# Performance work log

Measured on AMD Instinct MI355X. Metric: run time of the kernel, lower is better.

The kernel has to match this reference:

```python
import jax, jax.numpy as jnp
import numpy as np

B, S, E, H, FF = 4, 2048, 1024, 16, 4096
TD = 32  # transition_dim


def _layer_norm(v, g, b, eps=1e-5):
    m = v.mean(-1, keepdims=True)
    var = ((v - m) ** 2).mean(-1, keepdims=True)
    return (v - m) * jax.lax.rsqrt(var + eps) * g + b


def setup_inputs() -> dict:
    key = jax.random.key(0)
    ks = jax.random.split(key, 8)
    w = 0.02
    return {
        "x": jax.random.normal(ks[0], (B, S, E), dtype=jnp.float32),
        "transition_dim": TD,
        "ln1_g": jnp.ones((E,), jnp.float32),
        "ln1_b": jnp.zeros((E,), jnp.float32),
        "ln2_g": jnp.ones((E,), jnp.float32),
        "ln2_b": jnp.zeros((E,), jnp.float32),
        "w_qkv": jax.random.normal(ks[1], (3 * E, E), jnp.float32) * w,
        "b_qkv": jnp.zeros((3 * E,), jnp.float32),
        "w_o": jax.random.normal(ks[2], (E, E), jnp.float32) * w,
        "b_o": jnp.zeros((E,), jnp.float32),
        "w_fc1": jax.random.normal(ks[3], (FF, E), jnp.float32) * w,
        "b_fc1": jnp.zeros((FF,), jnp.float32),
        "w_fc2": jax.random.normal(ks[4], (E, FF), jnp.float32) * w,
        "b_fc2": jnp.zeros((E,), jnp.float32),
    }


def reference(x, transition_dim, ln1_g, ln1_b, ln2_g, ln2_b, w_qkv, b_qkv,
              w_o, b_o, w_fc1, b_fc1, w_fc2, b_fc2):
    Bx, Sx, Ex = x.shape
    Dh = Ex // H
    xn = _layer_norm(x, ln1_g, ln1_b)
    qkv = xn @ w_qkv.T + b_qkv                      # [B,S,3E]
    q, k, v = jnp.split(qkv, 3, axis=-1)
    def heads(t):
        return t.reshape(Bx, Sx, H, Dh).transpose(0, 2, 1, 3)  # [B,H,S,Dh]
    q, k, v = heads(q), heads(k), heads(v)
    scores = jnp.einsum("bhqd,bhkd->bhqk", q, k) / np.sqrt(Dh).astype(np.float32)
    # custom mask: causal (j > i) OR periodic value-column (j % TD == TD-1) blocked
    i = jnp.arange(Sx)
    mask = (i[None, :] > i[:, None]) | ((i[None, :] % transition_dim) == transition_dim - 1)
    scores = jnp.where(mask[None, None], -jnp.inf, scores)
    p = jax.nn.softmax(scores, axis=-1)
    attn = jnp.einsum("bhqk,bhkd->bhqd", p, v)
    attn = attn.transpose(0, 2, 1, 3).reshape(Bx, Sx, Ex)
    attn = attn @ w_o.T + b_o
    x = x + attn
    h = _layer_norm(x, ln2_g, ln2_b)
    h = jax.nn.gelu(h @ w_fc1.T + b_fc1, approximate=False) @ w_fc2.T + b_fc2
    return x + h
```

## Files before the change

### kernel.cpp

```cpp
#include <hip/hip_runtime.h>
#include <hip/hip_bf16.h>

typedef unsigned short u16;
typedef unsigned int u32;
typedef short bf16x8 __attribute__((ext_vector_type(8)));
typedef float f32x4 __attribute__((ext_vector_type(4)));
typedef float f32x16 __attribute__((ext_vector_type(16)));

#define B_ 4
#define S_ 2048
#define E_ 1024
#define H_ 16
#define FF_ 4096
#define M_ 8192

__device__ __forceinline__ u16 f2bf(float f) {
    u32 u = __float_as_uint(f);
    u32 r = (u + 0x7FFFu + ((u >> 16) & 1u)) >> 16;
    return (u16)r;
}
__device__ __forceinline__ float bf2f(u16 v) {
    return __uint_as_float(((u32)v) << 16);
}
__device__ __forceinline__ u32 cvtpk(float lo, float hi) {
    u32 r;
    asm("v_cvt_pk_bf16_f32 %0, %1, %2" : "=v"(r) : "v"(lo), "v"(hi));
    return r;
}
__device__ __forceinline__ void pswap(u32& a, u32& b) {
    asm("v_permlane32_swap_b32 %0, %1" : "+v"(a), "+v"(b));
}
__device__ __forceinline__ void gload16(const void* g, void* l) {
    __builtin_amdgcn_global_load_lds(
        (__attribute__((address_space(1))) void*)g,
        (__attribute__((address_space(3))) void*)l, 16, 0, 0);
}

__global__ __launch_bounds__(256) void cvt4_kernel(const float* __restrict__ s0, u16* __restrict__ d0,
                                                   const float* __restrict__ s1, u16* __restrict__ d1,
                                                   const float* __restrict__ s2, u16* __restrict__ d2,
                                                   const float* __restrict__ s3, u16* __restrict__ d3) {
    int blk = blockIdx.x;
    const float* s; u16* d; int base;
    if (blk < 3072)      { s = s0; d = d0; base = blk; }
    else if (blk < 4096) { s = s1; d = d1; base = blk - 3072; }
    else if (blk < 8192) { s = s2; d = d2; base = blk - 4096; }
    else                 { s = s3; d = d3; base = blk - 8192; }
    int i = base * 256 + threadIdx.x;
    float4 v = ((const float4*)s)[i];
    ushort4 o;
    o.x = f2bf(v.x); o.y = f2bf(v.y); o.z = f2bf(v.z); o.w = f2bf(v.w);
    ((ushort4*)d)[i] = o;
}

__global__ __launch_bounds__(256) void vtrans_kernel(const u16* __restrict__ qkv,
                                                     u16* __restrict__ vt) {
    __shared__ u16 tile[64 * 67];
    int t = threadIdx.x;
    int st = blockIdx.x;
    int bh = blockIdx.y;
    int b = bh >> 4, h = bh & 15;
    int s0 = st * 64;
    int r = t >> 3, c0 = (t & 7) * 8;
#pragma unroll
    for (int half = 0; half < 2; half++) {
        int rr = r + half * 32;
        const u16* src = qkv + (size_t)(b * S_ + s0 + rr) * 3072 + 2048 + h * 64 + c0;
        uint4 v = *(const uint4*)src;
        u16* pv = (u16*)&v;
#pragma unroll
        for (int e = 0; e < 8; e++) tile[(c0 + e) * 67 + rr] = pv[e];
    }
    __syncthreads();
    int d = t >> 2, ch = t & 3;
    u16 buf[16];
#pragma unroll
    for (int j = 0; j < 16; j++) buf[j] = tile[d * 67 + ch * 16 + j];
    u16* dst = vt + ((size_t)bh * 64 + d) * 2048 + s0 + ch * 16;
    *(uint4*)dst = *(uint4*)&buf[0];
    *(uint4*)(dst + 8) = *(uint4*)&buf[8];
}

__global__ __launch_bounds__(256) void ln_kernel(const float* __restrict__ x,
                                                 const float* __restrict__ g,
                                                 const float* __restrict__ bb,
                                                 u16* __restrict__ out) {
    int row = blockIdx.x;
    int t = threadIdx.x;
    const float4* xr = (const float4*)(x + (size_t)row * E_);
    float4 v = xr[t];
    float s = v.x + v.y + v.z + v.w;
    float sq = v.x * v.x + v.y * v.y + v.z * v.z + v.w * v.w;
    for (int o = 1; o < 64; o <<= 1) {
        s += __shfl_xor(s, o, 64);
        sq += __shfl_xor(sq, o, 64);
    }
    __shared__ float ss[4], sqs[4];
    int w = t >> 6, l = t & 63;
    if (l == 0) { ss[w] = s; sqs[w] = sq; }
    __syncthreads();
    s = ss[0] + ss[1] + ss[2] + ss[3];
    sq = sqs[0] + sqs[1] + sqs[2] + sqs[3];
    float mean = s * (1.0f / E_);
    float var = sq * (1.0f / E_) - mean * mean;
    float rstd = rsqrtf(var + 1e-5f);
    float4 gv = ((const float4*)g)[t];
    float4 bv = ((const float4*)bb)[t];
    ushort4 o4;
    o4.x = f2bf((v.x - mean) * rstd * gv.x + bv.x);
    o4.y = f2bf((v.y - mean) * rstd * gv.y + bv.y);
    o4.z = f2bf((v.z - mean) * rstd * gv.z + bv.z);
    o4.w = f2bf((v.w - mean) * rstd * gv.w + bv.w);
    ((ushort4*)(out + (size_t)row * E_))[t] = o4;
}

template <int EPI, int BN>
__global__ __launch_bounds__(512, 2) void gemm256(const u16* __restrict__ A,
                                                  const u16* __restrict__ Bt,
                                                  const float* __restrict__ bias,
                                                  void* __restrict__ outp,
                                                  const float* __restrict__ resid,
                                                  int N, int K) {
    constexpr int NF = BN / 64;
    __shared__ u16 ldsA[2 * 2 * 8192];
    __shared__ u16 ldsB[BN == 256 ? 2 * 2 * 8192 : 2 * 8192];
    int t = threadIdx.x;
    int wid = t >> 6, l = t & 63, l15 = l & 15, hi4 = l >> 4;
    int wm = wid >> 2, wn = wid & 3;

    int nwg = gridDim.x;
    int flat = blockIdx.x;
    int swz = (flat & 7) * (nwg >> 3) + (flat >> 3);
    int nx = N / BN;
    int m0 = (swz / nx) * 256, n0 = (swz % nx) * BN;
    const size_t Kb = (size_t)K * 2;

    f32x4 acc[8][NF];
    f32x4 zf = {0.f, 0.f, 0.f, 0.f};
#pragma unroll
    for (int i = 0; i < 8; i++)
#pragma unroll
        for (int j = 0; j < NF; j++) acc[i][j] = zf;

    auto stageA = [&](int buf, int h, int k0) {
#pragma unroll
        for (int rr = 0; rr < 2; ++rr) {
            int o = t * 16 + rr * 8192;
            int lr = o >> 7;
            int gch = ((o >> 4) & 7) ^ (lr & 7);
            int grow = m0 + (lr >> 6) * 128 + h * 64 + (lr & 63);
            gload16((const char*)A + (size_t)grow * Kb + k0 * 2 + gch * 16,
                    (char*)ldsA + (buf * 2 + h) * 16384 + o);
        }
    };
    auto stageB256 = [&](int buf, int h, int k0) {
#pragma unroll
        for (int rr = 0; rr < 2; ++rr) {
            int o = t * 16 + rr * 8192;
            int lr = o >> 7;
            int gch = ((o >> 4) & 7) ^ (lr & 7);
            int grow = n0 + (lr >> 5) * 64 + h * 32 + (lr & 31);
            gload16((const char*)Bt + (size_t)grow * Kb + k0 * 2 + gch * 16,
                    (char*)ldsB + (buf * 2 + h) * 16384 + o);
        }
    };
    auto stageB128 = [&](int buf, int k0) {
#pragma unroll
        for (int rr = 0; rr < 2; ++rr) {
            int o = t * 16 + rr * 8192;
            int lr = o >> 7;
            int gch = ((o >> 4) & 7) ^ (lr & 7);
            int grow = n0 + lr;
            gload16((const char*)Bt + (size_t)grow * Kb + k0 * 2 + gch * 16,
                    (char*)ldsB + buf * 16384 + o);
        }
    };

    auto readA = [&](int bq, int mh, bf16x8 (&af)[4][2]) {
#pragma unroll
        for (int mi = 0; mi < 4; mi++)
#pragma unroll
            for (int ks = 0; ks < 2; ks++) {
                int lr = wm * 64 + mi * 16 + l15;
                int ob = lr * 128 + ks * 64 + hi4 * 16;
                af[mi][ks] = *(const bf16x8*)((const char*)ldsA +
                             (bq * 2 + mh) * 16384 + (ob ^ ((lr & 7) << 4)));
            }
    };
    auto readB256 = [&](int bq, int nh, bf16x8 (&bfr)[2][2]) {
#pragma unroll
        for (int nq = 0; nq < 2; nq++)
#pragma unroll
            for (int ks = 0; ks < 2; ks++) {
                int lr = wn * 32 + nq * 16 + l15;
                int ob = lr * 128 + ks * 64 + hi4 * 16;
                bfr[nq][ks] = *(const bf16x8*)((const char*)ldsB +
                              (bq * 2 + nh) * 16384 + (ob ^ ((lr & 7) << 4)));
            }
    };
    auto readB128 = [&](int bq, bf16x8 (&bfr)[2][2]) {
#pragma unroll
        for (int nq = 0; nq < 2; nq++)
#pragma unroll
            for (int ks = 0; ks < 2; ks++) {
                int lr = wn * 32 + nq * 16 + l15;
                int ob = lr * 128 + ks * 64 + hi4 * 16;
                bfr[nq][ks] = *(const bf16x8*)((const char*)ldsB +
                              bq * 16384 + (ob ^ ((lr & 7) << 4)));
            }
    };
    auto mma = [&](bf16x8 (&af)[4][2], bf16x8 (&bfr)[2][2], int mh, int nh) {
#pragma unroll
        for (int mi = 0; mi < 4; mi++)
#pragma unroll
            for (int nq = 0; nq < 2; nq++)
#pragma unroll
                for (int ks = 0; ks < 2; ks++)
                    acc[mh * 4 + mi][nh * 2 + nq] =
                        __builtin_amdgcn_mfma_f32_16x16x32_bf16(
                            af[mi][ks], bfr[nq][ks], acc[mh * 4 + mi][nh * 2 + nq], 0, 0, 0);
    };

#define GWAIT(N)                                            \
    asm volatile("s_waitcnt vmcnt(" #N ")" ::: "memory");   \
    __builtin_amdgcn_sched_barrier(0);
#define PH_MID                                              \
    __builtin_amdgcn_s_barrier();                           \
    asm volatile("s_waitcnt lgkmcnt(0)" ::: "memory");      \
    __builtin_amdgcn_sched_barrier(0);                      \
    __builtin_amdgcn_s_setprio(1);
#define PH_END                                              \
    __builtin_amdgcn_s_setprio(0);                          \
    __builtin_amdgcn_s_barrier();

    int KT = K >> 6, ITERS = KT >> 1;

    if constexpr (BN == 256) {
        stageB256(0, 0, 0); stageB256(0, 1, 0); stageA(0, 0, 0); stageA(0, 1, 0);
        stageB256(1, 0, 64); stageB256(1, 1, 64); stageA(1, 0, 64);
        GWAIT(6);
        __builtin_amdgcn_s_barrier();
        for (int s = 0; s < ITERS; ++s) {
            int k1 = (2 * s + 1) << 6;
            int k2 = (2 * s + 2) << 6; if (k2 >= K) k2 = 0;
            int k3 = (2 * s + 3) << 6; if (k3 >= K) k3 = 0;
            bf16x8 af[4][2], b0[2][2], b1[2][2];
            readA(0, 0, af); readB256(0, 0, b0); stageA(1, 1, k1);
            PH_MID; mma(af, b0, 0, 0); PH_END;
            readB256(0, 1, b1); stageB256(0, 0, k2);
            PH_MID; mma(af, b1, 0, 1); PH_END;
            readA(0, 1, af); stageB256(0, 1, k2);
            PH_MID; mma(af, b0, 1, 0); PH_END;
            stageA(0, 0, k2); GWAIT(6);
            PH_MID; mma(af, b1, 1, 1); PH_END;
            readA(1, 0, af); readB256(1, 0, b0); stageA(0, 1, k2);
            PH_MID; mma(af, b0, 0, 0); PH_END;
            readB256(1, 1, b1); stageB256(1, 0, k3);
            PH_MID; mma(af, b1, 0, 1); PH_END;
            readA(1, 1, af); stageB256(1, 1, k3);
            PH_MID; mma(af, b0, 1, 0); PH_END;
            stageA(1, 0, k3); GWAIT(6);
            PH_MID; mma(af, b1, 1, 1); PH_END;
        }
    } else {
        stageB128(0, 0); stageA(0, 0, 0); stageA(0, 1, 0);
        stageB128(1, 64); stageA(1, 0, 64);
        GWAIT(4);
        __builtin_amdgcn_s_barrier();
        for (int s = 0; s < ITERS; ++s) {
            int k1 = (2 * s + 1) << 6;
            int k2 = (2 * s + 2) << 6; if (k2 >= K) k2 = 0;
            int k3 = (2 * s + 3) << 6; if (k3 >= K) k3 = 0;
            bf16x8 af[4][2], br[2][2];
            readA(0, 0, af); readB128(0, br); stageA(1, 1, k1);
            PH_MID; mma(af, br, 0, 0); PH_END;
            readA(0, 1, af); stageB128(0, k2); stageA(0, 0, k2); GWAIT(4);
            PH_MID; mma(af, br, 1, 0); PH_END;
            readA(1, 0, af); readB128(1, br); stageA(0, 1, k2);
            PH_MID; mma(af, br, 0, 0); PH_END;
            readA(1, 1, af); stageB128(1, k3); stageA(1, 0, k3); GWAIT(4);
            PH_MID; mma(af, br, 1, 0); PH_END;
        }
    }
#undef GWAIT
#undef PH_MID
#undef PH_END

    float bias_v[NF];
#pragma unroll
    for (int nf = 0; nf < NF; nf++) bias_v[nf] = bias[n0 + wn * (NF * 16) + nf * 16 + l15];

#pragma unroll
    for (int mf = 0; mf < 8; mf++)
#pragma unroll
        for (int nf = 0; nf < NF; nf++)
#pragma unroll
            for (int j = 0; j < 4; j++) {
                int row = m0 + wm * 128 + mf * 16 + hi4 * 4 + j;
                int col = n0 + wn * (NF * 16) + nf * 16 + l15;
                float v = acc[mf][nf][j] + bias_v[nf];
                size_t idx = (size_t)row * N + col;
                if (EPI == 2) v = 0.5f * v * (1.0f + erff(v * 0.70710678118f));
                if (EPI == 1)
                    ((float*)outp)[idx] = resid[idx] + v;
                else
                    ((u16*)outp)[idx] = f2bf(v);
            }
}

__global__ __launch_bounds__(128) void attn_kernel(const u16* __restrict__ qkv,
                                                   const u16* __restrict__ vt,
                                                   u16* __restrict__ aout) {
    __shared__ u16 Ksb[2 * 4096];
    __shared__ u16 Vsb[2 * 4096];
    int t = threadIdx.x;
    int wv = t >> 6, l = t & 63;
    int q31 = l & 31, hi = l >> 5;
    int flat = blockIdx.x;
    int logical = (flat & 7) * 128 + (flat >> 3);
    int bh = logical >> 4, p0 = logical & 15;
    int b = bh >> 4, h = bh & 15;

    const float qs = 0.18033688011f;
    const float THR = 44.3616f;

    const char* srcK0 = (const char*)(qkv + E_ + (size_t)(b * S_ + (t >> 3)) * 3072 + h * 64) +
                        ((t & 7) ^ ((t >> 3) & 7)) * 16;
    const char* srcV0 = (const char*)(vt + ((size_t)(bh * 64 + (t >> 3))) * 2048) +
                        ((t & 7) ^ ((t >> 3) & 7)) * 16;
    auto issueK = [&](int buf, int j0) {
#pragma unroll
        for (int pp = 0; pp < 4; pp++)
            gload16(srcK0 + (size_t)pp * 98304 + (size_t)j0 * 6144,
                    (char*)Ksb + buf * 8192 + 16 * t + 2048 * pp);
    };
    auto issueV = [&](int buf, int j0) {
#pragma unroll
        for (int pp = 0; pp < 4; pp++)
            gload16(srcV0 + (size_t)pp * 65536 + (size_t)j0 * 2,
                    (char*)Vsb + buf * 8192 + 16 * t + 2048 * pp);
    };

    f32x16 zf16;
#pragma unroll
    for (int r = 0; r < 16; r++) zf16[r] = 0.f;

    for (int half = 0; half < 2; ++half) {
        int qt = half ? (31 - p0) : p0;
        int rowq = qt * 64 + wv * 32 + q31;

        bf16x8 qreg[4];
        const u16* qbase = qkv + (size_t)(b * S_ + rowq) * 3072 + h * 64 + hi * 8;
#pragma unroll
        for (int g = 0; g < 4; g++) qreg[g] = *(const bf16x8*)(qbase + 16 * g);

        f32x16 o0 = zf16, o1 = zf16;
        float mrun = -INFINITY, lrun = 0.f;

        int j1 = (qt >= 1) ? 64 : 0;
        issueK(0, 0); issueV(0, 0);
        issueK(1, j1); issueV(1, j1);

        for (int jt = 0; jt <= qt; ++jt) {
            int cur = jt & 1;
            int j0 = jt * 64;
            asm volatile("s_waitcnt vmcnt(8)" ::: "memory");
            __builtin_amdgcn_sched_barrier(0);
            __builtin_amdgcn_s_barrier();

            const u16* Kc = Ksb + cur * 4096;
            const u16* Vc = Vsb + cur * 4096;

            f32x16 s0 = zf16, s1 = zf16;
            __builtin_amdgcn_s_setprio(1);
#pragma unroll
            for (int g = 0; g < 4; g++) {
                int r0 = q31, r1 = 32 + q31;
                bf16x8 k0 = *(const bf16x8*)&Kc[((r0 << 6) + hi * 8 + 16 * g) ^ ((r0 & 7) << 3)];
                bf16x8 k1 = *(const bf16x8*)&Kc[((r1 << 6) + hi * 8 + 16 * g) ^ ((r1 & 7) << 3)];
                s0 = __builtin_amdgcn_mfma_f32_32x32x16_bf16(k0, qreg[g], s0, 0, 0, 0);
                s1 = __builtin_amdgcn_mfma_f32_32x32x16_bf16(k1, qreg[g], s1, 0, 0, 0);
            }
            __builtin_amdgcn_s_setprio(0);

            float mx = -INFINITY;
            int cb0 = j0 + 4 * hi;
            if (jt == qt) {
#pragma unroll
                for (int r = 0; r < 16; r++) {
                    const int cc = (r & 3) + 8 * (r >> 2);
                    float v0 = s0[r], v1 = s1[r];
                    bool bad0 = (cb0 + cc > rowq) || (r == 15 && hi);
                    bool bad1 = (cb0 + 32 + cc > rowq) || (r == 15 && hi);
                    v0 = bad0 ? -INFINITY : v0;
                    v1 = bad1 ? -INFINITY : v1;
                    s0[r] = v0; s1[r] = v1;
                    mx = fmaxf(mx, fmaxf(v0, v1));
                }
            } else {
#pragma unroll
                for (int r = 0; r < 16; r++) {
                    float v0 = s0[r], v1 = s1[r];
                    if (r == 15) {
                        v0 = hi ? -INFINITY : v0;
                        v1 = hi ? -INFINITY : v1;
                        s0[r] = v0; s1[r] = v1;
                    }
                    mx = fmaxf(mx, fmaxf(v0, v1));
                }
            }
            mx = fmaxf(mx, __shfl_xor(mx, 32, 64));

            bool dokeep = __all(mx <= mrun + THR);
            if (!dokeep) {
                float mnew = fmaxf(mrun, mx);
                float sc = __builtin_amdgcn_exp2f((mrun - mnew) * qs);
#pragma unroll
                for (int r = 0; r < 16; r++) { o0[r] *= sc; o1[r] *= sc; }
                lrun *= sc;
                mrun = mnew;
            }
            float mq = mrun * qs;

            float sa = 0.f, sb = 0.f, sc2 = 0.f, sd = 0.f;
#pragma unroll
            for (int r = 0; r < 16; r++) {
                float p0 = __builtin_amdgcn_exp2f(fmaf(s0[r], qs, -mq));
                float p1 = __builtin_amdgcn_exp2f(fmaf(s1[r], qs, -mq));
                s0[r] = p0; s1[r] = p1;
                if (r & 1) { sb += p0; sd += p1; } else { sa += p0; sc2 += p1; }
            }
            lrun += (sa + sb) + (sc2 + sd);

            bf16x8 pa[4];
#pragma unroll
            for (int g = 0; g < 4; g++) {
                const int bs = (g & 1) * 8;
                u32 wa, wb, wc, wd;
                if (g < 2) {
                    wa = cvtpk(s0[bs + 0], s0[bs + 1]);
                    wb = cvtpk(s0[bs + 4], s0[bs + 5]);
                    wc = cvtpk(s0[bs + 2], s0[bs + 3]);
                    wd = cvtpk(s0[bs + 6], s0[bs + 7]);
                } else {
                    wa = cvtpk(s1[bs + 0], s1[bs + 1]);
                    wb = cvtpk(s1[bs + 4], s1[bs + 5]);
                    wc = cvtpk(s1[bs + 2], s1[bs + 3]);
                    wd = cvtpk(s1[bs + 6], s1[bs + 7]);
                }
                pswap(wa, wb);
                pswap(wc, wd);
                union { u32 w[4]; bf16x8 f; } u;
                u.w[0] = wa; u.w[1] = wc; u.w[2] = wb; u.w[3] = wd;
                pa[g] = u.f;
            }

            __builtin_amdgcn_s_setprio(1);
#pragma unroll
            for (int g = 0; g < 4; g++) {
                int d0 = q31, d1 = 32 + q31;
                bf16x8 v0 = *(const bf16x8*)&Vc[((d0 << 6) + hi * 8 + 16 * g) ^ ((d0 & 7) << 3)];
                bf16x8 v1 = *(const bf16x8*)&Vc[((d1 << 6) + hi * 8 + 16 * g) ^ ((d1 & 7) << 3)];
                o0 = __builtin_amdgcn_mfma_f32_32x32x16_bf16(v0, pa[g], o0, 0, 0, 0);
                o1 = __builtin_amdgcn_mfma_f32_32x32x16_bf16(v1, pa[g], o1, 0, 0, 0);
            }
            __builtin_amdgcn_s_setprio(0);

            __builtin_amdgcn_s_barrier();
            int nj = (jt + 2 <= qt) ? (jt + 2) * 64 : 0;
            issueK(cur, nj);
            issueV(cur, nj);
        }

        lrun += __shfl_xor(lrun, 32, 64);
        float inv = 1.0f / lrun;
        u16* orow = aout + (size_t)(b * S_ + rowq) * E_ + h * 64 + 4 * hi;
#pragma unroll
        for (int r = 0; r < 16; r++) {
            const int cc = (r & 3) + 8 * (r >> 2);
            orow[cc] = f2bf(o0[r] * inv);
            orow[32 + cc] = f2bf(o1[r] * inv);
        }

        if (half == 0) {
            asm volatile("s_waitcnt vmcnt(0)" ::: "memory");
            __builtin_amdgcn_sched_barrier(0);
            __builtin_amdgcn_s_barrier();
        }
    }
}

extern "C" void kernel_launch(void* const* d_in, const int* in_sizes, int n_in,
                              void* d_out, int out_size, void* d_ws, size_t ws_size,
                              hipStream_t stream) {
    const float* x = (const float*)d_in[0];
    const float* ln1_g = (const float*)d_in[2];
    const float* ln1_b = (const float*)d_in[3];
    const float* ln2_g = (const float*)d_in[4];
    const float* ln2_b = (const float*)d_in[5];
    const float* w_qkv = (const float*)d_in[6];
    const float* b_qkv = (const float*)d_in[7];
    const float* w_o = (const float*)d_in[8];
    const float* b_o = (const float*)d_in[9];
    const float* w_fc1 = (const float*)d_in[10];
    const float* b_fc1 = (const float*)d_in[11];
    const float* w_fc2 = (const float*)d_in[12];
    const float* b_fc2 = (const float*)d_in[13];
    float* out = (float*)d_out;
    char* ws = (char*)d_ws;

    u16* wqkv_bf = (u16*)(ws);
    u16* wo_bf   = (u16*)(ws + 6291456);
    u16* wfc1_bf = (u16*)(ws + 8388608);
    u16* wfc2_bf = (u16*)(ws + 16777216);
    u16* xn_bf   = (u16*)(ws + 25165824);
    u16* qkv_bf  = (u16*)(ws + 41943040);
    u16* ffn1_bf = (u16*)(ws + 41943040);
    u16* attn_bf = (u16*)(ws + 92274688);
    float* x2    = (float*)(ws + 109051904);
    u16* vtw     = (u16*)(ws + 109051904);
    (void)in_sizes; (void)n_in; (void)out_size; (void)ws_size;

    cvt4_kernel<<<12288, 256, 0, stream>>>(w_qkv, wqkv_bf, w_o, wo_bf,
                                           w_fc1, wfc1_bf, w_fc2, wfc2_bf);

    ln_kernel<<<M_, 256, 0, stream>>>(x, ln1_g, ln1_b, xn_bf);

    gemm256<0, 128><<<768, 512, 0, stream>>>(xn_bf, wqkv_bf, b_qkv, qkv_bf, nullptr, 3072, 1024);

    vtrans_kernel<<<dim3(32, 64), 256, 0, stream>>>(qkv_bf, vtw);

    attn_kernel<<<1024, 128, 0, stream>>>(qkv_bf, vtw, attn_bf);

    gemm256<1, 128><<<256, 512, 0, stream>>>(attn_bf, wo_bf, b_o, x2, x, 1024, 1024);

    ln_kernel<<<M_, 256, 0, stream>>>(x2, ln2_g, ln2_b, xn_bf);

    gemm256<2, 128><<<1024, 512, 0, stream>>>(xn_bf, wfc1_bf, b_fc1, ffn1_bf, nullptr, 4096, 1024);

    gemm256<1, 128><<<256, 512, 0, stream>>>(ffn1_bf, wfc2_bf, b_fc2, out, x2, 1024, 4096);
}
```

Baseline: 405.4 us.

## Add 128x128-tile GEMM kernel for QKV and FC1 projections

Adds a new 256-thread GEMM with 128x128 tiles, a simple double-buffered K loop and 4 waves. The QKV and FC1 GEMMs now use it, doubling the grid so more workgroups are in flight and wave quantization is lower on the CUs. The old 256-row kernel is specialized to BN=128 for the output-projection and FC2 GEMMs, with the unused BN=256 path removed. The smaller tiles give less data reuse per loaded byte and a less elaborate load/compute interleave.

```diff
diff --git a/kernel.cpp b/kernel.cpp
--- a/kernel.cpp
+++ b/kernel.cpp
@@ -114,16 +114,134 @@
     ((ushort4*)(out + (size_t)row * E_))[t] = o4;
 }
 
-template <int EPI, int BN>
-__global__ __launch_bounds__(512, 2) void gemm256(const u16* __restrict__ A,
-                                                  const u16* __restrict__ Bt,
-                                                  const float* __restrict__ bias,
-                                                  void* __restrict__ outp,
-                                                  const float* __restrict__ resid,
-                                                  int N, int K) {
-    constexpr int NF = BN / 64;
+template <int EPI>
+__global__ __launch_bounds__(256) void gemm128(const u16* __restrict__ A,
+                                               const u16* __restrict__ Bt,
+                                               const float* __restrict__ bias,
+                                               void* __restrict__ outp,
+                                               const float* __restrict__ resid,
+                                               int N, int K) {
+    __shared__ u16 ldsA[2 * 8192];
+    __shared__ u16 ldsB[2 * 8192];
+    int t = threadIdx.x;
+    int wid = t >> 6, l = t & 63, l15 = l & 15, hi4 = l >> 4;
+    int wm = wid >> 1, wn = wid & 1;
+
+    int nwg = gridDim.x;
+    int flat = blockIdx.x;
+    int swz = (flat & 7) * (nwg >> 3) + (flat >> 3);
+    int nx = N >> 7;
+    int m0 = (swz / nx) * 128, n0 = (swz % nx) * 128;
+    const size_t Kb = (size_t)K * 2;
+
+    f32x4 acc[4][4];
+    f32x4 zf = {0.f, 0.f, 0.f, 0.f};
+#pragma unroll
+    for (int i = 0; i < 4; i++)
+#pragma unroll
+        for (int j = 0; j < 4; j++) acc[i][j] = zf;
+
+    auto stageA = [&](int buf, int k0) {
+#pragma unroll
+        for (int rr = 0; rr < 4; ++rr) {
+            int o = t * 16 + rr * 4096;
+            int lr = o >> 7;
+            int gch = ((o >> 4) & 7) ^ (lr & 7);
+            gload16((const char*)A + (size_t)(m0 + lr) * Kb + k0 * 2 + gch * 16,
+                    (char*)ldsA + buf * 16384 + o);
+        }
+    };
+    auto stageB = [&](int buf, int k0) {
+#pragma unroll
+        for (int rr = 0; rr < 4; ++rr) {
+            int o = t * 16 + rr * 4096;
+            int lr = o >> 7;
+            int gch = ((o >> 4) & 7) ^ (lr & 7);
+            gload16((const char*)Bt + (size_t)(n0 + lr) * Kb + k0 * 2 + gch * 16,
+                    (char*)ldsB + buf * 16384 + o);
+        }
+    };
+
+    int NT = K >> 6;
+    stageA(0, 0); stageB(0, 0);
+    stageA(1, 64); stageB(1, 64);
+
+    for (int tt = 0; tt < NT; ++tt) {
+        int c = tt & 1;
+        asm volatile("s_waitcnt vmcnt(8)" ::: "memory");
+        __builtin_amdgcn_sched_barrier(0);
+        __builtin_amdgcn_s_barrier();
+
+        bf16x8 af[4][2], bf[4][2];
+#pragma unroll
+        for (int mi = 0; mi < 4; mi++)
+#pragma unroll
+            for (int ks = 0; ks < 2; ks++) {
+                int lr = wm * 64 + mi * 16 + l15;
+                int ob = lr * 128 + ks * 64 + hi4 * 16;
+                af[mi][ks] = *(const bf16x8*)((const char*)ldsA + c * 16384 +
+                                              (ob ^ ((lr & 7) << 4)));
+            }
+#pragma unroll
+        for (int nq = 0; nq < 4; nq++)
+#pragma unroll
+            for (int ks = 0; ks < 2; ks++) {
+                int lr = wn * 64 + nq * 16 + l15;
+                int ob = lr * 128 + ks * 64 + hi4 * 16;
+                bf[nq][ks] = *(const bf16x8*)((const char*)ldsB + c * 16384 +
+                                              (ob ^ ((lr & 7) << 4)));
+            }
+        asm volatile("s_waitcnt lgkmcnt(0)" ::: "memory");
+        __builtin_amdgcn_sched_barrier(0);
+        __builtin_amdgcn_s_setprio(1);
+#pragma unroll
+        for (int mi = 0; mi < 4; mi++)
+#pragma unroll
+            for (int nq = 0; nq < 4; nq++)
+#pragma unroll
+                for (int ks = 0; ks < 2; ks++)
+                    acc[mi][nq] = __builtin_amdgcn_mfma_f32_16x16x32_bf16(
+                        af[mi][ks], bf[nq][ks], acc[mi][nq], 0, 0, 0);
+        __builtin_amdgcn_s_setprio(0);
+        __builtin_amdgcn_s_barrier();
+
+        int kn = (tt + 2) * 64; if (kn >= K) kn = 0;
+        stageA(c, kn); stageB(c, kn);
+    }
+    asm volatile("s_waitcnt vmcnt(0)" ::: "memory");
+    __builtin_amdgcn_sched_barrier(0);
+
+    float bias_v[4];
+#pragma unroll
+    for (int nq = 0; nq < 4; nq++) bias_v[nq] = bias[n0 + wn * 64 + nq * 16 + l15];
+
+#pragma unroll
+    for (int mi = 0; mi < 4; mi++)
+#pragma unroll
+        for (int nq = 0; nq < 4; nq++)
+#pragma unroll
+            for (int j = 0; j < 4; j++) {
+                int row = m0 + wm * 64 + mi * 16 + hi4 * 4 + j;
+                int col = n0 + wn * 64 + nq * 16 + l15;
+                float v = acc[mi][nq][j] + bias_v[nq];
+                size_t idx = (size_t)row * N + col;
+                if (EPI == 2) v = 0.5f * v * (1.0f + erff(v * 0.70710678118f));
+                if (EPI == 1)
+                    ((float*)outp)[idx] = resid[idx] + v;
+                else
+                    ((u16*)outp)[idx] = f2bf(v);
+            }
+}
+
+template <int EPI>
+__global__ __launch_bounds__(512, 2) void gemm256n128(const u16* __restrict__ A,
+                                                      const u16* __restrict__ Bt,
+                                                      const float* __restrict__ bias,
+                                                      void* __restrict__ outp,
+                                                      const float* __restrict__ resid,
+                                                      int N, int K) {
     __shared__ u16 ldsA[2 * 2 * 8192];
-    __shared__ u16 ldsB[BN == 256 ? 2 * 2 * 8192 : 2 * 8192];
+    __shared__ u16 ldsB[2 * 8192];
     int t = threadIdx.x;
     int wid = t >> 6, l = t & 63, l15 = l & 15, hi4 = l >> 4;
     int wm = wid >> 2, wn = wid & 3;
@@ -131,16 +249,16 @@
     int nwg = gridDim.x;
     int flat = blockIdx.x;
     int swz = (flat & 7) * (nwg >> 3) + (flat >> 3);
-    int nx = N / BN;
-    int m0 = (swz / nx) * 256, n0 = (swz % nx) * BN;
+    int nx = N >> 7;
+    int m0 = (swz / nx) * 256, n0 = (swz % nx) * 128;
     const size_t Kb = (size_t)K * 2;
 
-    f32x4 acc[8][NF];
+    f32x4 acc[8][2];
     f32x4 zf = {0.f, 0.f, 0.f, 0.f};
 #pragma unroll
     for (int i = 0; i < 8; i++)
 #pragma unroll
-        for (int j = 0; j < NF; j++) acc[i][j] = zf;
+        for (int j = 0; j < 2; j++) acc[i][j] = zf;
 
     auto stageA = [&](int buf, int h, int k0) {
 #pragma unroll
@@ -153,18 +271,7 @@
                     (char*)ldsA + (buf * 2 + h) * 16384 + o);
         }
     };
-    auto stageB256 = [&](int buf, int h, int k0) {
-#pragma unroll
-        for (int rr = 0; rr < 2; ++rr) {
-            int o = t * 16 + rr * 8192;
-            int lr = o >> 7;
-            int gch = ((o >> 4) & 7) ^ (lr & 7);
-            int grow = n0 + (lr >> 5) * 64 + h * 32 + (lr & 31);
-            gload16((const char*)Bt + (size_t)grow * Kb + k0 * 2 + gch * 16,
-                    (char*)ldsB + (buf * 2 + h) * 16384 + o);
-        }
-    };
-    auto stageB128 = [&](int buf, int k0) {
+    auto stageB = [&](int buf, int k0) {
 #pragma unroll
         for (int rr = 0; rr < 2; ++rr) {
             int o = t * 16 + rr * 8192;
@@ -187,18 +294,7 @@
                              (bq * 2 + mh) * 16384 + (ob ^ ((lr & 7) << 4)));
             }
     };
-    auto readB256 = [&](int bq, int nh, bf16x8 (&bfr)[2][2]) {
-#pragma unroll
-        for (int nq = 0; nq < 2; nq++)
-#pragma unroll
-            for (int ks = 0; ks < 2; ks++) {
-                int lr = wn * 32 + nq * 16 + l15;
-                int ob = lr * 128 + ks * 64 + hi4 * 16;
-                bfr[nq][ks] = *(const bf16x8*)((const char*)ldsB +
-                              (bq * 2 + nh) * 16384 + (ob ^ ((lr & 7) << 4)));
-            }
-    };
-    auto readB128 = [&](int bq, bf16x8 (&bfr)[2][2]) {
+    auto readB = [&](int bq, bf16x8 (&bfr)[2][2]) {
 #pragma unroll
         for (int nq = 0; nq < 2; nq++)
 #pragma unroll
@@ -209,16 +305,16 @@
                               bq * 16384 + (ob ^ ((lr & 7) << 4)));
             }
     };
-    auto mma = [&](bf16x8 (&af)[4][2], bf16x8 (&bfr)[2][2], int mh, int nh) {
+    auto mma = [&](bf16x8 (&af)[4][2], bf16x8 (&bfr)[2][2], int mh) {
 #pragma unroll
         for (int mi = 0; mi < 4; mi++)
 #pragma unroll
             for (int nq = 0; nq < 2; nq++)
 #pragma unroll
                 for (int ks = 0; ks < 2; ks++)
-                    acc[mh * 4 + mi][nh * 2 + nq] =
+                    acc[mh * 4 + mi][nq] =
                         __builtin_amdgcn_mfma_f32_16x16x32_bf16(
-                            af[mi][ks], bfr[nq][ks], acc[mh * 4 + mi][nh * 2 + nq], 0, 0, 0);
+                            af[mi][ks], bfr[nq][ks], acc[mh * 4 + mi][nq], 0, 0, 0);
     };
 
 #define GWAIT(N)                                            \
@@ -233,72 +329,42 @@
     __builtin_amdgcn_s_setprio(0);                          \
     __builtin_amdgcn_s_barrier();
 
-    int KT = K >> 6, ITERS = KT >> 1;
-
-    if constexpr (BN == 256) {
-        stageB256(0, 0, 0); stageB256(0, 1, 0); stageA(0, 0, 0); stageA(0, 1, 0);
-        stageB256(1, 0, 64); stageB256(1, 1, 64); stageA(1, 0, 64);
-        GWAIT(6);
-        __builtin_amdgcn_s_barrier();
-        for (int s = 0; s < ITERS; ++s) {
-            int k1 = (2 * s + 1) << 6;
-            int k2 = (2 * s + 2) << 6; if (k2 >= K) k2 = 0;
-            int k3 = (2 * s + 3) << 6; if (k3 >= K) k3 = 0;
-            bf16x8 af[4][2], b0[2][2], b1[2][2];
-            readA(0, 0, af); readB256(0, 0, b0); stageA(1, 1, k1);
-            PH_MID; mma(af, b0, 0, 0); PH_END;
-            readB256(0, 1, b1); stageB256(0, 0, k2);
-            PH_MID; mma(af, b1, 0, 1); PH_END;
-            readA(0, 1, af); stageB256(0, 1, k2);
-            PH_MID; mma(af, b0, 1, 0); PH_END;
-            stageA(0, 0, k2); GWAIT(6);
-            PH_MID; mma(af, b1, 1, 1); PH_END;
-            readA(1, 0, af); readB256(1, 0, b0); stageA(0, 1, k2);
-            PH_MID; mma(af, b0, 0, 0); PH_END;
-            readB256(1, 1, b1); stageB256(1, 0, k3);
-            PH_MID; mma(af, b1, 0, 1); PH_END;
-            readA(1, 1, af); stageB256(1, 1, k3);
-            PH_MID; mma(af, b0, 1, 0); PH_END;
-            stageA(1, 0, k3); GWAIT(6);
-            PH_MID; mma(af, b1, 1, 1); PH_END;
-        }
-    } else {
-        stageB128(0, 0); stageA(0, 0, 0); stageA(0, 1, 0);
-        stageB128(1, 64); stageA(1, 0, 64);
-        GWAIT(4);
-        __builtin_amdgcn_s_barrier();
-        for (int s = 0; s < ITERS; ++s) {
-            int k1 = (2 * s + 1) << 6;
-            int k2 = (2 * s + 2) << 6; if (k2 >= K) k2 = 0;
-            int k3 = (2 * s + 3) << 6; if (k3 >= K) k3 = 0;
-            bf16x8 af[4][2], br[2][2];
-            readA(0, 0, af); readB128(0, br); stageA(1, 1, k1);
-            PH_MID; mma(af, br, 0, 0); PH_END;
-            readA(0, 1, af); stageB128(0, k2); stageA(0, 0, k2); GWAIT(4);
-            PH_MID; mma(af, br, 1, 0); PH_END;
-            readA(1, 0, af); readB128(1, br); stageA(0, 1, k2);
-            PH_MID; mma(af, br, 0, 0); PH_END;
-            readA(1, 1, af); stageB128(1, k3); stageA(1, 0, k3); GWAIT(4);
-            PH_MID; mma(af, br, 1, 0); PH_END;
-        }
+    int ITERS = K >> 7;
+    stageB(0, 0); stageA(0, 0, 0); stageA(0, 1, 0);
+    stageB(1, 64); stageA(1, 0, 64);
+    GWAIT(4);
+    __builtin_amdgcn_s_barrier();
+    for (int s = 0; s < ITERS; ++s) {
+        int k1 = (2 * s + 1) << 6;
+        int k2 = (2 * s + 2) << 6; if (k2 >= K) k2 = 0;
+        int k3 = (2 * s + 3) << 6; if (k3 >= K) k3 = 0;
+        bf16x8 af[4][2], br[2][2];
+        readA(0, 0, af); readB(0, br); stageA(1, 1, k1);
+        PH_MID; mma(af, br, 0); PH_END;
+        readA(0, 1, af); stageB(0, k2); stageA(0, 0, k2); GWAIT(4);
+        PH_MID; mma(af, br, 1); PH_END;
+        readA(1, 0, af); readB(1, br); stageA(0, 1, k2);
+        PH_MID; mma(af, br, 0); PH_END;
+        readA(1, 1, af); stageB(1, k3); stageA(1, 0, k3); GWAIT(4);
+        PH_MID; mma(af, br, 1); PH_END;
     }
 #undef GWAIT
 #undef PH_MID
 #undef PH_END
 
-    float bias_v[NF];
-#pragma unroll
-    for (int nf = 0; nf < NF; nf++) bias_v[nf] = bias[n0 + wn * (NF * 16) + nf * 16 + l15];
+    float bias_v[2];
+#pragma unroll
+    for (int nq = 0; nq < 2; nq++) bias_v[nq] = bias[n0 + wn * 32 + nq * 16 + l15];
 
 #pragma unroll
     for (int mf = 0; mf < 8; mf++)
 #pragma unroll
-        for (int nf = 0; nf < NF; nf++)
+        for (int nq = 0; nq < 2; nq++)
 #pragma unroll
             for (int j = 0; j < 4; j++) {
                 int row = m0 + wm * 128 + mf * 16 + hi4 * 4 + j;
-                int col = n0 + wn * (NF * 16) + nf * 16 + l15;
-                float v = acc[mf][nf][j] + bias_v[nf];
+                int col = n0 + wn * 32 + nq * 16 + l15;
+                float v = acc[mf][nq][j] + bias_v[nq];
                 size_t idx = (size_t)row * N + col;
                 if (EPI == 2) v = 0.5f * v * (1.0f + erff(v * 0.70710678118f));
                 if (EPI == 1)
@@ -526,17 +592,17 @@
 
     ln_kernel<<<M_, 256, 0, stream>>>(x, ln1_g, ln1_b, xn_bf);
 
-    gemm256<0, 128><<<768, 512, 0, stream>>>(xn_bf, wqkv_bf, b_qkv, qkv_bf, nullptr, 3072, 1024);
+    gemm128<0><<<1536, 256, 0, stream>>>(xn_bf, wqkv_bf, b_qkv, qkv_bf, nullptr, 3072, 1024);
 
     vtrans_kernel<<<dim3(32, 64), 256, 0, stream>>>(qkv_bf, vtw);
 
     attn_kernel<<<1024, 128, 0, stream>>>(qkv_bf, vtw, attn_bf);
 
-    gemm256<1, 128><<<256, 512, 0, stream>>>(attn_bf, wo_bf, b_o, x2, x, 1024, 1024);
+    gemm256n128<1><<<256, 512, 0, stream>>>(attn_bf, wo_bf, b_o, x2, x, 1024, 1024);
 
     ln_kernel<<<M_, 256, 0, stream>>>(x2, ln2_g, ln2_b, xn_bf);
 
-    gemm256<2, 128><<<1024, 512, 0, stream>>>(xn_bf, wfc1_bf, b_fc1, ffn1_bf, nullptr, 4096, 1024);
-
-    gemm256<1, 128><<<256, 512, 0, stream>>>(ffn1_bf, wfc2_bf, b_fc2, out, x2, 1024, 4096);
-}
+    gemm128<2><<<2048, 256, 0, stream>>>(xn_bf, wfc1_bf, b_fc1, ffn1_bf, nullptr, 4096, 1024);
+
+    gemm256n128<1><<<256, 512, 0, stream>>>(ffn1_bf, wfc2_bf, b_fc2, out, x2, 1024, 4096);
+}
```

Result: faster. 393.3 us (-3.0%).
